# Performance work log

Hardware: AMD Instinct MI355X
Metric: run time of the kernel (lower is better)

The kernel has to match this reference:

```python
import jax, jax.numpy as jnp
import numpy as np

# ---- config (mirrors argparse-config of dnc_model) ----
T, B, IN = 64, 32, 64          # time-major input [T,B,IN]
N, Wd, R, NW = 512, 64, 4, 1   # memory_size, word_size, num_reads, num_writes
H, OUT = 256, 64               # controller hidden, output_size
CLIP = 20.0
EPS = 1e-6
IF = R*Wd + R + NW*Wd + NW + NW*Wd + NW*Wd + R + NW + NW + R*(1+2*NW)  # interface size = 471
CTRL_IN = IN + R*Wd


def setup_inputs() -> dict:
    key = jax.random.key(0)
    ks = jax.random.split(key, 6)
    g = lambda k, shape, s: (jax.random.normal(k, shape, jnp.float32) * s)
    return {
        "inputs": g(ks[0], (T, B, IN), 1.0),
        "Wx": g(ks[1], (CTRL_IN, 4*H), 0.05),
        "Wh": g(ks[2], (H, 4*H), 0.05),
        "b_lstm": jnp.zeros((4*H,), jnp.float32),
        "W_if": g(ks[3], (H, IF), 0.05),
        "b_if": jnp.zeros((IF,), jnp.float32),
        "W_out": g(ks[4], (H + R*Wd, OUT), 0.05),
        "b_out": jnp.zeros((OUT,), jnp.float32),
    }


def _clip(x):
    return jnp.clip(x, -CLIP, CLIP)


def _oneplus(x):
    return 1.0 + jax.nn.softplus(x)


def _content_weights(memory, keys, strengths):
    # memory [B,N,Wd], keys [B,K,Wd], strengths [B,K] -> softmax cosine weights [B,K,N]
    dot = jnp.einsum('bkw,bnw->bkn', keys, memory)
    mn = jnp.sqrt(jnp.sum(memory * memory, -1))          # [B,N]
    kn = jnp.sqrt(jnp.sum(keys * keys, -1))              # [B,K]
    sim = dot / (kn[..., None] * mn[:, None, :] + EPS)
    return jax.nn.softmax(sim * strengths[..., None], axis=-1)


def _allocation(usage):
    # usage [B,N] -> allocation weights [B,N] (sorted-free-list scheme)
    u = EPS + (1.0 - EPS) * usage
    idx = jnp.argsort(u, axis=-1)                        # ascending usage
    su = jnp.take_along_axis(u, idx, -1)
    cp = jnp.cumprod(su, axis=-1)
    excl = jnp.concatenate([jnp.ones_like(cp[:, :1]), cp[:, :-1]], -1)
    a_sorted = (1.0 - su) * excl
    inv = jnp.argsort(idx, axis=-1)
    return jnp.take_along_axis(a_sorted, inv, -1)


def _dnc_forward(inputs, Wx, Wh, b_lstm, W_if, b_if, W_out, b_out):
    eye = jnp.eye(N, dtype=inputs.dtype)

    def step(carry, x_t):
        h, c, mem, rw, ww_prev, link, prec, usage, reads = carry
        # ---- controller LSTM (prev read vectors fed in) ----
        ctrl_in = jnp.concatenate([x_t, reads.reshape(B, R*Wd)], -1)
        gates = ctrl_in @ Wx + h @ Wh + b_lstm
        ig, fg, gg, og = jnp.split(gates, 4, -1)
        c = jax.nn.sigmoid(fg) * c + jax.nn.sigmoid(ig) * jnp.tanh(gg)
        h = jax.nn.sigmoid(og) * jnp.tanh(c)
        hc, cc = _clip(h), _clip(c)
        # ---- interface vector ----
        itf = hc @ W_if + b_if
        off = 0
        read_keys = itf[:, off:off+R*Wd].reshape(B, R, Wd); off += R*Wd
        read_str = _oneplus(itf[:, off:off+R]); off += R
        write_keys = itf[:, off:off+NW*Wd].reshape(B, NW, Wd); off += NW*Wd
        write_str = _oneplus(itf[:, off:off+NW]); off += NW
        erase = jax.nn.sigmoid(itf[:, off:off+NW*Wd]).reshape(B, NW, Wd); off += NW*Wd
        write_vecs = itf[:, off:off+NW*Wd].reshape(B, NW, Wd); off += NW*Wd
        free_g = jax.nn.sigmoid(itf[:, off:off+R]); off += R
        alloc_g = jax.nn.sigmoid(itf[:, off:off+NW]); off += NW
        write_g = jax.nn.sigmoid(itf[:, off:off+NW]); off += NW
        modes = jax.nn.softmax(itf[:, off:off+R*(1+2*NW)].reshape(B, R, 1+2*NW), -1)
        bwd_mode = modes[..., :NW]
        fwd_mode = modes[..., NW:2*NW]
        content_mode = modes[..., 2*NW]
        # ---- usage update (uses prev write/read weights) ----
        u = usage + (1.0 - usage) * (1.0 - jnp.prod(1.0 - ww_prev, axis=1))
        psi = jnp.prod(1.0 - free_g[..., None] * rw, axis=1)
        usage = u * psi
        # ---- write weights: allocation + content ----
        allocs = []
        u_run = usage
        for hd in range(NW):
            a = _allocation(u_run)
            allocs.append(a)
            u_run = u_run + (1.0 - u_run) * (write_g[:, hd:hd+1] * alloc_g[:, hd:hd+1]) * a
        alloc = jnp.stack(allocs, 1)                      # [B,NW,N]
        wc = _content_weights(mem, write_keys, write_str) # [B,NW,N]
        ww = write_g[..., None] * (alloc_g[..., None] * alloc + (1.0 - alloc_g[..., None]) * wc)
        # ---- erase / add write ----
        erase_w = ww[..., None] * erase[:, :, None, :]    # [B,NW,N,Wd]
        mem = mem * jnp.prod(1.0 - erase_w, axis=1) + jnp.einsum('bhn,bhw->bnw', ww, write_vecs)
        # ---- temporal link + precedence ----
        w_i = ww[..., :, None]
        w_j = ww[..., None, :]
        link = (1.0 - w_i - w_j) * link + w_i * prec[..., None, :]
        link = link * (1.0 - eye)
        prec = (1.0 - ww.sum(-1, keepdims=True)) * prec + ww
        # ---- read weights: content + forward/backward linkage ----
        rc = _content_weights(mem, read_keys, read_str)   # [B,R,N]
        fw = jnp.einsum('bhij,brj->brhi', link, rw)       # forward  [B,R,NW,N]
        bw = jnp.einsum('bhji,brj->brhi', link, rw)       # backward [B,R,NW,N]
        rw = (content_mode[..., None] * rc
              + jnp.einsum('brh,brhn->brn', fwd_mode, fw)
              + jnp.einsum('brh,brhn->brn', bwd_mode, bw))
        reads = jnp.einsum('brn,bnw->brw', rw, mem)       # [B,R,Wd]
        out = _clip(jnp.concatenate([hc, reads.reshape(B, R*Wd)], -1) @ W_out + b_out)
        return (hc, cc, mem, rw, ww, link, prec, usage, reads), out

    z = jnp.zeros
    dt = inputs.dtype
    carry0 = (z((B, H), dt), z((B, H), dt), z((B, N, Wd), dt), z((B, R, N), dt),
              z((B, NW, N), dt), z((B, NW, N, N), dt), z((B, NW, N), dt),
              z((B, N), dt), z((B, R, Wd), dt))
    _, outs = jax.lax.scan(step, carry0, inputs)
    return outs  # [T, B, OUT]


def reference(inputs, Wx, Wh, b_lstm, W_if, b_if, W_out, b_out):
    return _dnc_forward(inputs, Wx, Wh, b_lstm, W_if, b_if, W_out, b_out)
```

## Files before the change

### kernel.cpp

```cpp
#include <hip/hip_runtime.h>
#include <math.h>

#define Tn 64
#define Bn 32
#define INn 64
#define Nn 512
#define WDn 64
#define Rn 4
#define Hn 256
#define G4H 1024
#define OUTn 64
#define IFn 471
#define CLIPV 20.0f
#define EPSV 1e-6f

#define OFF_RKEY 0
#define OFF_RSTR 256
#define OFF_WKEY 260
#define OFF_WSTR 324
#define OFF_ERASE 325
#define OFF_WVEC 389
#define OFF_FREE 453
#define OFF_AG 457
#define OFF_WG 458
#define OFF_MODES 459

__device__ float S_h[2][Bn][Hn];
__device__ float S_c[2][Bn][Hn];
__device__ float S_gates[2][Bn][G4H];
__device__ float S_mem[Bn][Nn][WDn];
__device__ float S_rw[Bn][Rn][Nn];
__device__ float S_ww[2][Bn][Nn];
__device__ float S_link[Bn][Nn][Nn];
__device__ float S_prec[2][Bn][Nn];
__device__ float S_usage[2][Bn][Nn];
__device__ float S_reads[Bn][Rn][WDn];
__device__ float S_itf[Bn][IFn];
__device__ float S_rc[Bn][Rn][Nn];
__device__ float S_fw[Bn][Rn][Nn];
__device__ float S_bwp[Bn][8][Rn*Nn];
__device__ float S_sumww[Bn];
__device__ unsigned int g_ww[Bn];
__device__ unsigned int g_rc[Bn];
__device__ unsigned int g_ld[Bn];
__device__ unsigned int g_fin;

__device__ __forceinline__ float sigm(float x){ return 1.f/(1.f+expf(-x)); }
__device__ __forceinline__ float clipv(float x){ return fminf(fmaxf(x,-CLIPV),CLIPV); }
__device__ __forceinline__ float oneplusf(float x){
  float sp = (x > 0.f) ? (x + log1pf(expf(-x))) : log1pf(expf(x));
  return 1.f + sp;
}
__device__ __forceinline__ float wredsum(float v){
  #pragma unroll
  for (int o=32;o>0;o>>=1) v += __shfl_xor(v,o,64);
  return v;
}
__device__ __forceinline__ float bredsum(float v, volatile float* scr){
  v = wredsum(v);
  if ((threadIdx.x & 63) == 0) scr[threadIdx.x >> 6] = v;
  __syncthreads();
  float s = scr[0];
  #pragma unroll
  for (int i=1;i<8;i++) s += scr[i];
  __syncthreads();
  return s;
}
__device__ __forceinline__ float bredmax(float v, volatile float* scr){
  #pragma unroll
  for (int o=32;o>0;o>>=1) v = fmaxf(v,__shfl_xor(v,o,64));
  if ((threadIdx.x & 63) == 0) scr[threadIdx.x >> 6] = v;
  __syncthreads();
  float m = scr[0];
  #pragma unroll
  for (int i=1;i<8;i++) m = fmaxf(m, scr[i]);
  __syncthreads();
  return m;
}
__device__ __forceinline__ void sig_release(unsigned int* flag){
  __builtin_amdgcn_fence(__ATOMIC_RELEASE, "agent");
  __hip_atomic_fetch_add(flag, 1u, __ATOMIC_RELAXED, __HIP_MEMORY_SCOPE_AGENT);
}
__device__ __forceinline__ void spin_until(unsigned int* flag, unsigned int target){
  while (__hip_atomic_load(flag, __ATOMIC_RELAXED, __HIP_MEMORY_SCOPE_AGENT) < target)
    __builtin_amdgcn_s_sleep(8);
}

extern "C" __global__ void __launch_bounds__(256)
k_init(){
  size_t g = (size_t)blockIdx.x*256 + threadIdx.x;
  size_t stride = (size_t)gridDim.x*256;
  float* lk = &S_link[0][0][0];
  for (size_t i=g; i<(size_t)Bn*Nn*Nn; i+=stride) lk[i]=0.f;
  float* mm = &S_mem[0][0][0];
  for (size_t i=g; i<(size_t)Bn*Nn*WDn; i+=stride) mm[i]=0.f;
  float* rr = &S_rw[0][0][0];
  for (size_t i=g; i<(size_t)Bn*Rn*Nn; i+=stride) rr[i]=0.f;
  float* rd = &S_reads[0][0][0];
  for (size_t i=g; i<(size_t)Bn*Rn*WDn; i+=stride) rd[i]=0.f;
  for (size_t i=g; i<(size_t)2*Bn*Nn; i+=stride){
    S_ww[0][0][i]=0.f; S_prec[0][0][i]=0.f; S_usage[0][0][i]=0.f;
  }
  for (size_t i=g; i<(size_t)2*Bn*Hn; i+=stride){
    S_h[0][0][i]=0.f; S_c[0][0][i]=0.f;
  }
  if (blockIdx.x==0){
    if (threadIdx.x < Bn){ g_ww[threadIdx.x]=0u; g_rc[threadIdx.x]=0u; g_ld[threadIdx.x]=0u; }
    if (threadIdx.x == 0) g_fin=0u;
  }
}

struct ShG { float ctrl[Bn][65]; };

__device__ __forceinline__ void gates_core(ShG& sg, int tn, int jt,
        const float* __restrict__ xin, const float* __restrict__ Wx,
        const float* __restrict__ Wh, const float* __restrict__ b_lstm){
  const int tid = threadIdx.x, lane = tid & 63, wvi = tid >> 6;
  const int j = jt*64 + lane;
  const int hp = (tn+1)&1;
  const int b0 = wvi*4;
  float bias = b_lstm[j];
  float a0=bias, a1=bias, a2=bias, a3=bias;
  for (int c=0;c<9;++c){
    #pragma unroll
    for (int u=0;u<4;u++){
      int e = u*512 + tid;
      int b2 = e >> 6, kk = e & 63;
      float v;
      if (c==0)       v = xin[((size_t)tn*Bn + b2)*INn + kk];
      else if (c<5)   v = ((const float*)S_reads[b2])[(c-1)*64 + kk];
      else            v = S_h[hp][b2][(c-5)*64 + kk];
      sg.ctrl[b2][kk] = v;
    }
    __syncthreads();
    const float* wb = (c<5) ? (Wx + (size_t)(c*64)*G4H + j)
                            : (Wh + (size_t)((c-5)*64)*G4H + j);
    #pragma unroll
    for (int kk=0;kk<64;kk++){
      float wv = wb[(size_t)kk*G4H];
      a0 += sg.ctrl[b0+0][kk]*wv;
      a1 += sg.ctrl[b0+1][kk]*wv;
      a2 += sg.ctrl[b0+2][kk]*wv;
      a3 += sg.ctrl[b0+3][kk]*wv;
    }
    __syncthreads();
  }
  const int gs = tn&1;
  S_gates[gs][b0+0][j]=a0;
  S_gates[gs][b0+1][j]=a1;
  S_gates[gs][b0+2][j]=a2;
  S_gates[gs][b0+3][j]=a3;
}

extern "C" __global__ void __launch_bounds__(512)
k_gates_pro(const float* __restrict__ xin, const float* __restrict__ Wx,
            const float* __restrict__ Wh, const float* __restrict__ b_lstm){
  __shared__ ShG sg;
  gates_core(sg, 0, blockIdx.x, xin, Wx, Wh, b_lstm);
}

struct ShA {
  float hc[Hn];
  float itf[IFn];
  unsigned long long keys[Nn];
  float alloc[Nn];
  float sim[Nn];
  float rsim[Rn][Nn];
  float tile[64][65];
  float wkey[WDn];
  float rk[Rn][WDn];
  float er[WDn];
  float wv[WDn];
  float red[8];
  float knw, knr[Rn], betar[Rn];
};
struct ShL {
  float ww[Nn];
  float prec[Nn];
  float rw[Rn][Nn];
  float bwp4[4][Rn][Nn];
};
struct ShF {
  float fw[Rn][Nn];
  float bw[Rn][Nn];
  float rc[Rn][Nn];
  float modes[Rn][4];
  float part[8][Rn][WDn];
  float vin[512];
};
union ShU { ShA a; ShL l; ShF f; ShG g; };

extern "C" __global__ void __launch_bounds__(512, 4)
k_step(int t, const float* __restrict__ xin,
       const float* __restrict__ Wx, const float* __restrict__ Wh,
       const float* __restrict__ b_lstm,
       const float* __restrict__ W_if, const float* __restrict__ b_if,
       const float* __restrict__ W_out, const float* __restrict__ b_out,
       float* __restrict__ outp){
  __shared__ ShU sh;
  const int tid = threadIdx.x;
  const int lane = tid & 63, wvi = tid >> 6;
  const int bid = blockIdx.x;
  const int cur = t&1, prev = cur^1;

  if (bid < 32){
    const int b = bid;
    if (tid < Hn){
      int h = tid;
      float g0=S_gates[cur][b][h],     g1=S_gates[cur][b][Hn+h];
      float g2=S_gates[cur][b][2*Hn+h],g3=S_gates[cur][b][3*Hn+h];
      float cold = S_c[prev][b][h];
      float cn = sigm(g1)*cold + sigm(g0)*tanhf(g2);
      float hn = sigm(g3)*tanhf(cn);
      float hcv = clipv(hn);
      S_c[cur][b][h] = clipv(cn);
      S_h[cur][b][h] = hcv;
      sh.a.hc[h] = hcv;
    }
    __syncthreads();
    if (tid < IFn){
      float acc = b_if[tid];
      for (int k=0;k<Hn;k+=8){
        float s = 0.f;
        #pragma unroll
        for (int u=0;u<8;u++) s += sh.a.hc[k+u]*W_if[(size_t)(k+u)*IFn + tid];
        acc += s;
      }
      sh.a.itf[tid] = acc;
      S_itf[b][tid] = acc;
    }
    __syncthreads();
    if (tid < WDn){
      sh.a.wkey[tid] = sh.a.itf[OFF_WKEY+tid];
      sh.a.er[tid]   = sigm(sh.a.itf[OFF_ERASE+tid]);
      sh.a.wv[tid]   = sh.a.itf[OFF_WVEC+tid];
    } else if (tid < WDn + Rn*WDn){
      int k2 = tid - WDn;
      sh.a.rk[k2>>6][k2&63] = sh.a.itf[OFF_RKEY + k2];
    }
    {
      float fg0=sigm(sh.a.itf[OFF_FREE+0]), fg1=sigm(sh.a.itf[OFF_FREE+1]);
      float fg2=sigm(sh.a.itf[OFF_FREE+2]), fg3=sigm(sh.a.itf[OFF_FREE+3]);
      int n = tid;
      float uu = S_usage[prev][b][n], wwp = S_ww[prev][b][n];
      float u = uu + (1.f-uu)*wwp;
      float psi = (1.f - fg0*S_rw[b][0][n])*(1.f - fg1*S_rw[b][1][n])
                * (1.f - fg2*S_rw[b][2][n])*(1.f - fg3*S_rw[b][3][n]);
      float un = u*psi;
      S_usage[cur][b][n] = un;
      float v = EPSV + (1.f-EPSV)*un;
      sh.a.keys[n] = ((unsigned long long)__float_as_uint(v) << 32) | (unsigned)n;
    }
    __syncthreads();
    if (wvi==0){
      float kv = sh.a.wkey[lane];
      float s2 = wredsum(kv*kv);
      if (lane==0) sh.a.knw = sqrtf(s2);
    } else if (wvi<=4){
      int r = wvi-1;
      float kv = sh.a.rk[r][lane];
      float s2 = wredsum(kv*kv);
      if (lane==0) sh.a.knr[r] = sqrtf(s2);
    } else if (wvi==5 && lane<4){
      sh.a.betar[lane] = oneplusf(sh.a.itf[OFF_RSTR+lane]);
    }
    {
      unsigned long long myk = sh.a.keys[tid];
      float prod = 1.f;
      for (int j=0;j<Nn;j+=8){
        #pragma unroll
        for (int u=0;u<8;u++){
          unsigned long long kj = sh.a.keys[j+u];
          float uj = __uint_as_float((unsigned)(kj>>32));
          prod *= (kj < myk) ? uj : 1.f;
        }
      }
      float myu = __uint_as_float((unsigned)(myk>>32));
      sh.a.alloc[tid] = (1.f - myu)*prod;
    }
    __syncthreads();
    float betaw = oneplusf(sh.a.itf[OFF_WSTR]);
    for (int tile=0;tile<8;tile++){
      #pragma unroll
      for (int u=0;u<8;u++){
        int e = u*512 + tid;
        int nn = e>>6, w = e&63;
        sh.a.tile[nn][w] = S_mem[b][tile*64+nn][w];
      }
      __syncthreads();
      {
        int nn = tid>>3, qq = tid&7;
        float d=0.f, nrm=0.f;
        #pragma unroll
        for (int i=0;i<8;i++){
          int w = qq*8+i;
          float m = sh.a.tile[nn][w];
          d += m*sh.a.wkey[w]; nrm += m*m;
        }
        #pragma unroll
        for (int o=1;o<8;o<<=1){ d += __shfl_xor(d,o,64); nrm += __shfl_xor(nrm,o,64); }
        if (qq==0){
          int n = tile*64+nn;
          sh.a.sim[n] = betaw * d / (sh.a.knw*sqrtf(nrm) + EPSV);
        }
      }
      __syncthreads();
    }
    {
      float v = sh.a.sim[tid];
      float mx = bredmax(v, sh.a.red);
      float e = expf(v - mx);
      float ssum = bredsum(e, sh.a.red);
      float wc = e/ssum;
      float ag = sigm(sh.a.itf[OFF_AG]);
      float wg = sigm(sh.a.itf[OFF_WG]);
      float wwv = wg*(ag*sh.a.alloc[tid] + (1.f-ag)*wc);
      S_ww[cur][b][tid] = wwv;
      float wsum = bredsum(wwv, sh.a.red);
      if (tid==0) S_sumww[b] = wsum;
      sh.a.alloc[tid] = wwv;
    }
    __syncthreads();
    if (tid==0) sig_release(&g_ww[b]);
    for (int tile=0;tile<8;tile++){
      #pragma unroll
      for (int u=0;u<8;u++){
        int e = u*512 + tid;
        int nn = e>>6, w = e&63;
        int n = tile*64+nn;
        float m = S_mem[b][n][w];
        float wwn = sh.a.alloc[n];
        m = m*(1.f - wwn*sh.a.er[w]) + wwn*sh.a.wv[w];
        S_mem[b][n][w] = m;
        sh.a.tile[nn][w] = m;
      }
      __syncthreads();
      {
        int nn = tid>>3, qq = tid&7;
        float a0=0.f,a1=0.f,a2=0.f,a3=0.f,nrm=0.f;
        #pragma unroll
        for (int i=0;i<8;i++){
          int w = qq*8+i;
          float m = sh.a.tile[nn][w];
          a0 += m*sh.a.rk[0][w]; a1 += m*sh.a.rk[1][w];
          a2 += m*sh.a.rk[2][w]; a3 += m*sh.a.rk[3][w];
          nrm += m*m;
        }
        #pragma unroll
        for (int o=1;o<8;o<<=1){
          a0 += __shfl_xor(a0,o,64); a1 += __shfl_xor(a1,o,64);
          a2 += __shfl_xor(a2,o,64); a3 += __shfl_xor(a3,o,64);
          nrm += __shfl_xor(nrm,o,64);
        }
        if (qq==0){
          int n = tile*64+nn;
          float mn = sqrtf(nrm);
          sh.a.rsim[0][n] = sh.a.betar[0]*a0/(sh.a.knr[0]*mn + EPSV);
          sh.a.rsim[1][n] = sh.a.betar[1]*a1/(sh.a.knr[1]*mn + EPSV);
          sh.a.rsim[2][n] = sh.a.betar[2]*a2/(sh.a.knr[2]*mn + EPSV);
          sh.a.rsim[3][n] = sh.a.betar[3]*a3/(sh.a.knr[3]*mn + EPSV);
        }
      }
      __syncthreads();
    }
    for (int r=0;r<Rn;r++){
      float v = sh.a.rsim[r][tid];
      float mx = bredmax(v, sh.a.red);
      float e = expf(v - mx);
      float ssum = bredsum(e, sh.a.red);
      S_rc[b][r][tid] = e/ssum;
    }
    __syncthreads();
    if (tid==0) sig_release(&g_rc[b]);

  } else if (bid < 288){
    const int idx = bid - 32;
    const int b = idx >> 3, ch = idx & 7;
    const int i0 = ch*64;
    if (tid==0){
      spin_until(&g_ww[b], (unsigned)(t+1));
      __builtin_amdgcn_fence(__ATOMIC_ACQUIRE, "agent");
    }
    __syncthreads();
    sh.l.ww[tid]   = S_ww[cur][b][tid];
    sh.l.prec[tid] = S_prec[prev][b][tid];
    for (int k=tid;k<Rn*Nn;k+=512) ((float*)sh.l.rw)[k] = ((const float*)S_rw[b])[k];
    __syncthreads();
    float sumww = S_sumww[b];
    float wj[2][4], pj[2][4], rj[4][2][4];
    #pragma unroll
    for (int jjc=0;jjc<2;jjc++){
      float4 w4 = ((const float4*)sh.l.ww)[jjc*64+lane];
      float4 p4 = ((const float4*)sh.l.prec)[jjc*64+lane];
      wj[jjc][0]=w4.x; wj[jjc][1]=w4.y; wj[jjc][2]=w4.z; wj[jjc][3]=w4.w;
      pj[jjc][0]=p4.x; pj[jjc][1]=p4.y; pj[jjc][2]=p4.z; pj[jjc][3]=p4.w;
      #pragma unroll
      for (int r=0;r<4;r++){
        float4 r4 = ((const float4*)sh.l.rw[r])[jjc*64+lane];
        rj[r][jjc][0]=r4.x; rj[r][jjc][1]=r4.y; rj[r][jjc][2]=r4.z; rj[r][jjc][3]=r4.w;
      }
    }
    float bwa[4][2][4];
    #pragma unroll
    for (int r=0;r<4;r++)
      #pragma unroll
      for (int jjc=0;jjc<2;jjc++)
        #pragma unroll
        for (int s=0;s<4;s++) bwa[r][jjc][s]=0.f;
    for (int rr=0;rr<8;rr++){
      const int i = i0 + wvi*8 + rr;
      float wi = sh.l.ww[i];
      float ci = 1.f - wi;
      float ri[4] = {sh.l.rw[0][i], sh.l.rw[1][i], sh.l.rw[2][i], sh.l.rw[3][i]};
      float f[4] = {0.f,0.f,0.f,0.f};
      float4* lrow4 = (float4*)(&S_link[b][i][0]);
      #pragma unroll
      for (int jjc=0;jjc<2;jjc++){
        float4 L4 = lrow4[jjc*64+lane];
        float Ls[4] = {L4.x, L4.y, L4.z, L4.w};
        #pragma unroll
        for (int s=0;s<4;s++){
          float Ln = (ci - wj[jjc][s])*Ls[s] + wi*pj[jjc][s];
          int j = jjc*256 + lane*4 + s;
          Ln = (j==i) ? 0.f : Ln;
          Ls[s] = Ln;
          #pragma unroll
          for (int r=0;r<4;r++){
            f[r] += Ln*rj[r][jjc][s];
            bwa[r][jjc][s] += Ln*ri[r];
          }
        }
        float4 Lo; Lo.x=Ls[0]; Lo.y=Ls[1]; Lo.z=Ls[2]; Lo.w=Ls[3];
        lrow4[jjc*64+lane] = Lo;
      }
      #pragma unroll
      for (int r=0;r<4;r++){
        float fr = wredsum(f[r]);
        if (lane==0) S_fw[b][r][i] = fr;
      }
    }
    if (wvi < 4){
      #pragma unroll
      for (int r=0;r<4;r++)
        #pragma unroll
        for (int jjc=0;jjc<2;jjc++){
          float4 v4; v4.x=bwa[r][jjc][0]; v4.y=bwa[r][jjc][1]; v4.z=bwa[r][jjc][2]; v4.w=bwa[r][jjc][3];
          ((float4*)sh.l.bwp4[wvi][r])[jjc*64+lane] = v4;
        }
    }
    __syncthreads();
    if (wvi >= 4){
      int v = wvi-4;
      #pragma unroll
      for (int r=0;r<4;r++)
        #pragma unroll
        for (int jjc=0;jjc<2;jjc++){
          float4 v4 = ((float4*)sh.l.bwp4[v][r])[jjc*64+lane];
          v4.x+=bwa[r][jjc][0]; v4.y+=bwa[r][jjc][1]; v4.z+=bwa[r][jjc][2]; v4.w+=bwa[r][jjc][3];
          ((float4*)sh.l.bwp4[v][r])[jjc*64+lane] = v4;
        }
    }
    __syncthreads();
    for (int k=tid;k<Rn*Nn;k+=512){
      float s = ((float*)sh.l.bwp4[0])[k] + ((float*)sh.l.bwp4[1])[k]
              + ((float*)sh.l.bwp4[2])[k] + ((float*)sh.l.bwp4[3])[k];
      S_bwp[b][ch][k] = s;
    }
    if (tid < 64){
      int j = i0 + tid;
      S_prec[cur][b][j] = (1.f - sumww)*sh.l.prec[j] + sh.l.ww[j];
    }
    __syncthreads();
    if (tid==0) sig_release(&g_ld[b]);

  } else if (bid < 320){
    const int b = bid - 288;
    if (tid==0){
      spin_until(&g_ld[b], 8u*(unsigned)(t+1));
      spin_until(&g_rc[b], (unsigned)(t+1));
      __builtin_amdgcn_fence(__ATOMIC_ACQUIRE, "agent");
    }
    __syncthreads();
    for (int k=tid;k<Rn*Nn;k+=512){
      ((float*)sh.f.fw)[k] = ((const float*)S_fw[b])[k];
      float sbw = 0.f;
      #pragma unroll
      for (int ch=0;ch<8;ch++) sbw += S_bwp[b][ch][k];
      ((float*)sh.f.bw)[k] = sbw;
      ((float*)sh.f.rc)[k] = ((const float*)S_rc[b])[k];
    }
    if (tid < 4){
      int r = tid;
      float m0 = S_itf[b][OFF_MODES + r*3 + 0];
      float m1 = S_itf[b][OFF_MODES + r*3 + 1];
      float m2 = S_itf[b][OFF_MODES + r*3 + 2];
      float mx = fmaxf(m0,fmaxf(m1,m2));
      float e0=expf(m0-mx), e1=expf(m1-mx), e2=expf(m2-mx);
      float si = e0+e1+e2;
      sh.f.modes[r][0]=e0/si; sh.f.modes[r][1]=e1/si; sh.f.modes[r][2]=e2/si;
    }
    __syncthreads();
    for (int k=tid;k<Rn*Nn;k+=512){
      int r = k>>9, n = k&511;
      float v = sh.f.modes[r][2]*sh.f.rc[r][n] + sh.f.modes[r][1]*sh.f.fw[r][n]
              + sh.f.modes[r][0]*sh.f.bw[r][n];
      sh.f.rc[r][n] = v;
      S_rw[b][r][n] = v;
    }
    __syncthreads();
    {
      float a0=0.f,a1=0.f,a2=0.f,a3=0.f;
      #pragma unroll 4
      for (int nn=0;nn<64;nn++){
        int n = wvi*64+nn;
        float m = S_mem[b][n][lane];
        a0 += sh.f.rc[0][n]*m; a1 += sh.f.rc[1][n]*m;
        a2 += sh.f.rc[2][n]*m; a3 += sh.f.rc[3][n]*m;
      }
      sh.f.part[wvi][0][lane]=a0; sh.f.part[wvi][1][lane]=a1;
      sh.f.part[wvi][2][lane]=a2; sh.f.part[wvi][3][lane]=a3;
    }
    __syncthreads();
    if (tid < 256){
      int r = tid>>6, w = tid&63;
      float sv = 0.f;
      #pragma unroll
      for (int v=0;v<8;v++) sv += sh.f.part[v][r][w];
      S_reads[b][r][w] = sv;
      sh.f.vin[256+tid] = sv;
      sh.f.vin[tid] = S_h[cur][b][tid];
    }
    __syncthreads();
    {
      int qq = tid>>6, o = tid&63;
      float sacc = 0.f;
      for (int k2=qq*64;k2<qq*64+64;k2+=8){
        #pragma unroll
        for (int u=0;u<8;u++) sacc += sh.f.vin[k2+u]*W_out[(size_t)(k2+u)*OUTn + o];
      }
      sh.f.part[qq][0][o] = sacc;
    }
    __syncthreads();
    if (tid < 64){
      float sv = b_out[tid];
      #pragma unroll
      for (int qq=0;qq<8;qq++) sv += sh.f.part[qq][0][tid];
      outp[((size_t)t*Bn + b)*OUTn + tid] = clipv(sv);
    }
    __syncthreads();
    if (tid==0) sig_release(&g_fin);

  } else {
    if (t+1 >= Tn) return;
    const int jt = bid - 320;
    if (tid==0){
      spin_until(&g_fin, 32u*(unsigned)(t+1));
      __builtin_amdgcn_fence(__ATOMIC_ACQUIRE, "agent");
    }
    __syncthreads();
    gates_core(sh.g, t+1, jt, xin, Wx, Wh, b_lstm);
  }
}

extern "C" void kernel_launch(void* const* d_in, const int* in_sizes, int n_in,
                              void* d_out, int out_size, void* d_ws, size_t ws_size,
                              hipStream_t stream){
  (void)in_sizes; (void)n_in; (void)d_ws; (void)ws_size; (void)out_size;
  const float* xin = (const float*)d_in[0];
  const float* Wx  = (const float*)d_in[1];
  const float* Wh  = (const float*)d_in[2];
  const float* bl  = (const float*)d_in[3];
  const float* Wif = (const float*)d_in[4];
  const float* bif = (const float*)d_in[5];
  const float* Wo  = (const float*)d_in[6];
  const float* bo  = (const float*)d_in[7];
  hipLaunchKernelGGL(k_init, dim3(1024), dim3(256), 0, stream);
  hipLaunchKernelGGL(k_gates_pro, dim3(16), dim3(512), 0, stream, xin, Wx, Wh, bl);
  for (int t=0; t<Tn; ++t){
    hipLaunchKernelGGL(k_step, dim3(336), dim3(512), 0, stream,
                       t, xin, Wx, Wh, bl, Wif, bif, Wo, bo, (float*)d_out);
  }
}
```

Before: 7.154 ms.

## Move memory write and read-content weights to final blocks, overlap gate precompute

The memory erase/write update and the read-content similarity softmax move out of the per-batch controller blocks into the final read blocks. Those blocks now start right after the write weights are published and run concurrently with the linkage blocks, instead of serialising behind them. The next-step gate blocks begin the x and h parts of the LSTM matmul as soon as a new h-published flag is set, deferring only the read-vector part until the step finishes. This shortens the critical path per step at the cost of more flags and more work in the read blocks. Flags are padded to separate cache lines, the spin sleep is shortened, and the W_if loop unroll is increased.

```diff
diff --git a/kernel.cpp b/kernel.cpp
--- a/kernel.cpp
+++ b/kernel.cpp
@@ -36,14 +36,13 @@
 __device__ float S_usage[2][Bn][Nn];
 __device__ float S_reads[Bn][Rn][WDn];
 __device__ float S_itf[Bn][IFn];
-__device__ float S_rc[Bn][Rn][Nn];
 __device__ float S_fw[Bn][Rn][Nn];
 __device__ float S_bwp[Bn][8][Rn*Nn];
 __device__ float S_sumww[Bn];
-__device__ unsigned int g_ww[Bn];
-__device__ unsigned int g_rc[Bn];
-__device__ unsigned int g_ld[Bn];
-__device__ unsigned int g_fin;
+__device__ unsigned int g_hh[16];
+__device__ unsigned int g_ww[Bn][16];
+__device__ unsigned int g_ld[Bn][16];
+__device__ unsigned int g_fin[16];
 
 __device__ __forceinline__ float sigm(float x){ return 1.f/(1.f+expf(-x)); }
 __device__ __forceinline__ float clipv(float x){ return fminf(fmaxf(x,-CLIPV),CLIPV); }
@@ -83,7 +82,14 @@
 }
 __device__ __forceinline__ void spin_until(unsigned int* flag, unsigned int target){
   while (__hip_atomic_load(flag, __ATOMIC_RELAXED, __HIP_MEMORY_SCOPE_AGENT) < target)
-    __builtin_amdgcn_s_sleep(8);
+    __builtin_amdgcn_s_sleep(4);
+}
+__device__ __forceinline__ void wait_acq1(unsigned int* f, unsigned int tgt){
+  if (threadIdx.x==0){
+    spin_until(f, tgt);
+    __builtin_amdgcn_fence(__ATOMIC_ACQUIRE, "agent");
+  }
+  __syncthreads();
 }
 
 extern "C" __global__ void __launch_bounds__(256)
@@ -105,19 +111,55 @@
     S_h[0][0][i]=0.f; S_c[0][0][i]=0.f;
   }
   if (blockIdx.x==0){
-    if (threadIdx.x < Bn){ g_ww[threadIdx.x]=0u; g_rc[threadIdx.x]=0u; g_ld[threadIdx.x]=0u; }
-    if (threadIdx.x == 0) g_fin=0u;
+    for (int i=threadIdx.x; i<16; i+=256){ g_hh[i]=0u; g_fin[i]=0u; }
+    for (int i=threadIdx.x; i<Bn*16; i+=256){
+      ((unsigned int*)g_ww)[i]=0u; ((unsigned int*)g_ld)[i]=0u;
+    }
   }
 }
 
 struct ShG { float ctrl[Bn][65]; };
-
-__device__ __forceinline__ void gates_core(ShG& sg, int tn, int jt,
-        const float* __restrict__ xin, const float* __restrict__ Wx,
-        const float* __restrict__ Wh, const float* __restrict__ b_lstm){
+struct ShA {
+  float hc[Hn];
+  float itf[IFn];
+  unsigned long long keys[Nn];
+  float alloc[Nn];
+  float sim[Nn];
+  float tile[64][65];
+  float wkey[WDn];
+  float red[8];
+  float knw;
+};
+struct ShL {
+  float ww[Nn];
+  float prec[Nn];
+  float rw[Rn][Nn];
+  float bwp4[4][Rn][Nn];
+};
+struct ShF {
+  float er[WDn];
+  float wv[WDn];
+  float rk[Rn][WDn];
+  float betar[Rn];
+  float knr[Rn];
+  float modes[Rn][4];
+  float ww[Nn];
+  float tile[64][65];
+  float rsim[Rn][Nn];
+  float fw[Rn][Nn];
+  float bw[Rn][Nn];
+  float part[8][Rn][WDn];
+  float vin[512];
+  float red[8];
+};
+union ShU { ShA a; ShL l; ShF f; ShG g; };
+
+extern "C" __global__ void __launch_bounds__(512)
+k_gates_pro(const float* __restrict__ xin, const float* __restrict__ Wx,
+            const float* __restrict__ Wh, const float* __restrict__ b_lstm){
+  __shared__ ShG sg;
   const int tid = threadIdx.x, lane = tid & 63, wvi = tid >> 6;
-  const int j = jt*64 + lane;
-  const int hp = (tn+1)&1;
+  const int j = blockIdx.x*64 + lane;
   const int b0 = wvi*4;
   float bias = b_lstm[j];
   float a0=bias, a1=bias, a2=bias, a3=bias;
@@ -127,9 +169,9 @@
       int e = u*512 + tid;
       int b2 = e >> 6, kk = e & 63;
       float v;
-      if (c==0)       v = xin[((size_t)tn*Bn + b2)*INn + kk];
-      else if (c<5)   v = ((const float*)S_reads[b2])[(c-1)*64 + kk];
-      else            v = S_h[hp][b2][(c-5)*64 + kk];
+      if (c==0)       v = xin[(size_t)b2*INn + kk];
+      else if (c<5)   v = 0.f;
+      else            v = 0.f;
       sg.ctrl[b2][kk] = v;
     }
     __syncthreads();
@@ -145,50 +187,11 @@
     }
     __syncthreads();
   }
-  const int gs = tn&1;
-  S_gates[gs][b0+0][j]=a0;
-  S_gates[gs][b0+1][j]=a1;
-  S_gates[gs][b0+2][j]=a2;
-  S_gates[gs][b0+3][j]=a3;
-}
-
-extern "C" __global__ void __launch_bounds__(512)
-k_gates_pro(const float* __restrict__ xin, const float* __restrict__ Wx,
-            const float* __restrict__ Wh, const float* __restrict__ b_lstm){
-  __shared__ ShG sg;
-  gates_core(sg, 0, blockIdx.x, xin, Wx, Wh, b_lstm);
-}
-
-struct ShA {
-  float hc[Hn];
-  float itf[IFn];
-  unsigned long long keys[Nn];
-  float alloc[Nn];
-  float sim[Nn];
-  float rsim[Rn][Nn];
-  float tile[64][65];
-  float wkey[WDn];
-  float rk[Rn][WDn];
-  float er[WDn];
-  float wv[WDn];
-  float red[8];
-  float knw, knr[Rn], betar[Rn];
-};
-struct ShL {
-  float ww[Nn];
-  float prec[Nn];
-  float rw[Rn][Nn];
-  float bwp4[4][Rn][Nn];
-};
-struct ShF {
-  float fw[Rn][Nn];
-  float bw[Rn][Nn];
-  float rc[Rn][Nn];
-  float modes[Rn][4];
-  float part[8][Rn][WDn];
-  float vin[512];
-};
-union ShU { ShA a; ShL l; ShF f; ShG g; };
+  S_gates[0][b0+0][j]=a0;
+  S_gates[0][b0+1][j]=a1;
+  S_gates[0][b0+2][j]=a2;
+  S_gates[0][b0+3][j]=a3;
+}
 
 extern "C" __global__ void __launch_bounds__(512, 4)
 k_step(int t, const float* __restrict__ xin,
@@ -218,26 +221,20 @@
       sh.a.hc[h] = hcv;
     }
     __syncthreads();
+    if (tid==0) sig_release(&g_hh[0]);
     if (tid < IFn){
       float acc = b_if[tid];
-      for (int k=0;k<Hn;k+=8){
+      for (int k=0;k<Hn;k+=16){
         float s = 0.f;
         #pragma unroll
-        for (int u=0;u<8;u++) s += sh.a.hc[k+u]*W_if[(size_t)(k+u)*IFn + tid];
+        for (int u=0;u<16;u++) s += sh.a.hc[k+u]*W_if[(size_t)(k+u)*IFn + tid];
         acc += s;
       }
       sh.a.itf[tid] = acc;
       S_itf[b][tid] = acc;
     }
     __syncthreads();
-    if (tid < WDn){
-      sh.a.wkey[tid] = sh.a.itf[OFF_WKEY+tid];
-      sh.a.er[tid]   = sigm(sh.a.itf[OFF_ERASE+tid]);
-      sh.a.wv[tid]   = sh.a.itf[OFF_WVEC+tid];
-    } else if (tid < WDn + Rn*WDn){
-      int k2 = tid - WDn;
-      sh.a.rk[k2>>6][k2&63] = sh.a.itf[OFF_RKEY + k2];
-    }
+    if (tid < WDn) sh.a.wkey[tid] = sh.a.itf[OFF_WKEY+tid];
     {
       float fg0=sigm(sh.a.itf[OFF_FREE+0]), fg1=sigm(sh.a.itf[OFF_FREE+1]);
       float fg2=sigm(sh.a.itf[OFF_FREE+2]), fg3=sigm(sh.a.itf[OFF_FREE+3]);
@@ -256,13 +253,6 @@
       float kv = sh.a.wkey[lane];
       float s2 = wredsum(kv*kv);
       if (lane==0) sh.a.knw = sqrtf(s2);
-    } else if (wvi<=4){
-      int r = wvi-1;
-      float kv = sh.a.rk[r][lane];
-      float s2 = wredsum(kv*kv);
-      if (lane==0) sh.a.knr[r] = sqrtf(s2);
-    } else if (wvi==5 && lane<4){
-      sh.a.betar[lane] = oneplusf(sh.a.itf[OFF_RSTR+lane]);
     }
     {
       unsigned long long myk = sh.a.keys[tid];
@@ -318,70 +308,15 @@
       S_ww[cur][b][tid] = wwv;
       float wsum = bredsum(wwv, sh.a.red);
       if (tid==0) S_sumww[b] = wsum;
-      sh.a.alloc[tid] = wwv;
-    }
-    __syncthreads();
-    if (tid==0) sig_release(&g_ww[b]);
-    for (int tile=0;tile<8;tile++){
-      #pragma unroll
-      for (int u=0;u<8;u++){
-        int e = u*512 + tid;
-        int nn = e>>6, w = e&63;
-        int n = tile*64+nn;
-        float m = S_mem[b][n][w];
-        float wwn = sh.a.alloc[n];
-        m = m*(1.f - wwn*sh.a.er[w]) + wwn*sh.a.wv[w];
-        S_mem[b][n][w] = m;
-        sh.a.tile[nn][w] = m;
-      }
-      __syncthreads();
-      {
-        int nn = tid>>3, qq = tid&7;
-        float a0=0.f,a1=0.f,a2=0.f,a3=0.f,nrm=0.f;
-        #pragma unroll
-        for (int i=0;i<8;i++){
-          int w = qq*8+i;
-          float m = sh.a.tile[nn][w];
-          a0 += m*sh.a.rk[0][w]; a1 += m*sh.a.rk[1][w];
-          a2 += m*sh.a.rk[2][w]; a3 += m*sh.a.rk[3][w];
-          nrm += m*m;
-        }
-        #pragma unroll
-        for (int o=1;o<8;o<<=1){
-          a0 += __shfl_xor(a0,o,64); a1 += __shfl_xor(a1,o,64);
-          a2 += __shfl_xor(a2,o,64); a3 += __shfl_xor(a3,o,64);
-          nrm += __shfl_xor(nrm,o,64);
-        }
-        if (qq==0){
-          int n = tile*64+nn;
-          float mn = sqrtf(nrm);
-          sh.a.rsim[0][n] = sh.a.betar[0]*a0/(sh.a.knr[0]*mn + EPSV);
-          sh.a.rsim[1][n] = sh.a.betar[1]*a1/(sh.a.knr[1]*mn + EPSV);
-          sh.a.rsim[2][n] = sh.a.betar[2]*a2/(sh.a.knr[2]*mn + EPSV);
-          sh.a.rsim[3][n] = sh.a.betar[3]*a3/(sh.a.knr[3]*mn + EPSV);
-        }
-      }
-      __syncthreads();
-    }
-    for (int r=0;r<Rn;r++){
-      float v = sh.a.rsim[r][tid];
-      float mx = bredmax(v, sh.a.red);
-      float e = expf(v - mx);
-      float ssum = bredsum(e, sh.a.red);
-      S_rc[b][r][tid] = e/ssum;
-    }
-    __syncthreads();
-    if (tid==0) sig_release(&g_rc[b]);
+    }
+    __syncthreads();
+    if (tid==0) sig_release(&g_ww[b][0]);
 
   } else if (bid < 288){
     const int idx = bid - 32;
     const int b = idx >> 3, ch = idx & 7;
     const int i0 = ch*64;
-    if (tid==0){
-      spin_until(&g_ww[b], (unsigned)(t+1));
-      __builtin_amdgcn_fence(__ATOMIC_ACQUIRE, "agent");
-    }
-    __syncthreads();
+    wait_acq1(&g_ww[b][0], (unsigned)(t+1));
     sh.l.ww[tid]   = S_ww[cur][b][tid];
     sh.l.prec[tid] = S_prec[prev][b][tid];
     for (int k=tid;k<Rn*Nn;k+=512) ((float*)sh.l.rw)[k] = ((const float*)S_rw[b])[k];
@@ -471,26 +406,22 @@
       S_prec[cur][b][j] = (1.f - sumww)*sh.l.prec[j] + sh.l.ww[j];
     }
     __syncthreads();
-    if (tid==0) sig_release(&g_ld[b]);
+    if (tid==0) sig_release(&g_ld[b][0]);
 
   } else if (bid < 320){
     const int b = bid - 288;
-    if (tid==0){
-      spin_until(&g_ld[b], 8u*(unsigned)(t+1));
-      spin_until(&g_rc[b], (unsigned)(t+1));
-      __builtin_amdgcn_fence(__ATOMIC_ACQUIRE, "agent");
-    }
-    __syncthreads();
-    for (int k=tid;k<Rn*Nn;k+=512){
-      ((float*)sh.f.fw)[k] = ((const float*)S_fw[b])[k];
-      float sbw = 0.f;
-      #pragma unroll
-      for (int ch=0;ch<8;ch++) sbw += S_bwp[b][ch][k];
-      ((float*)sh.f.bw)[k] = sbw;
-      ((float*)sh.f.rc)[k] = ((const float*)S_rc[b])[k];
-    }
-    if (tid < 4){
-      int r = tid;
+    wait_acq1(&g_ww[b][0], (unsigned)(t+1));
+    if (tid < WDn){
+      sh.f.er[tid] = sigm(S_itf[b][OFF_ERASE+tid]);
+      sh.f.wv[tid] = S_itf[b][OFF_WVEC+tid];
+    } else if (tid < WDn + Rn*WDn){
+      int k2 = tid - WDn;
+      sh.f.rk[k2>>6][k2&63] = S_itf[b][OFF_RKEY + k2];
+    } else if (tid < WDn + Rn*WDn + Rn){
+      int r = tid - (WDn+Rn*WDn);
+      sh.f.betar[r] = oneplusf(S_itf[b][OFF_RSTR + r]);
+    } else if (tid >= 384 && tid < 384+Rn){
+      int r = tid - 384;
       float m0 = S_itf[b][OFF_MODES + r*3 + 0];
       float m1 = S_itf[b][OFF_MODES + r*3 + 1];
       float m2 = S_itf[b][OFF_MODES + r*3 + 2];
@@ -499,12 +430,76 @@
       float si = e0+e1+e2;
       sh.f.modes[r][0]=e0/si; sh.f.modes[r][1]=e1/si; sh.f.modes[r][2]=e2/si;
     }
+    sh.f.ww[tid] = S_ww[cur][b][tid];
+    __syncthreads();
+    if (wvi < 4){
+      float kv = sh.f.rk[wvi][lane];
+      float s2 = wredsum(kv*kv);
+      if (lane==0) sh.f.knr[wvi] = sqrtf(s2);
+    }
+    for (int tile=0;tile<8;tile++){
+      #pragma unroll
+      for (int u=0;u<8;u++){
+        int e = u*512 + tid;
+        int nn = e>>6, w = e&63;
+        int n = tile*64+nn;
+        float m = S_mem[b][n][w];
+        float wwn = sh.f.ww[n];
+        m = m*(1.f - wwn*sh.f.er[w]) + wwn*sh.f.wv[w];
+        S_mem[b][n][w] = m;
+        sh.f.tile[nn][w] = m;
+      }
+      __syncthreads();
+      {
+        int nn = tid>>3, qq = tid&7;
+        float a0=0.f,a1=0.f,a2=0.f,a3=0.f,nrm=0.f;
+        #pragma unroll
+        for (int i=0;i<8;i++){
+          int w = qq*8+i;
+          float m = sh.f.tile[nn][w];
+          a0 += m*sh.f.rk[0][w]; a1 += m*sh.f.rk[1][w];
+          a2 += m*sh.f.rk[2][w]; a3 += m*sh.f.rk[3][w];
+          nrm += m*m;
+        }
+        #pragma unroll
+        for (int o=1;o<8;o<<=1){
+          a0 += __shfl_xor(a0,o,64); a1 += __shfl_xor(a1,o,64);
+          a2 += __shfl_xor(a2,o,64); a3 += __shfl_xor(a3,o,64);
+          nrm += __shfl_xor(nrm,o,64);
+        }
+        if (qq==0){
+          int n = tile*64+nn;
+          float mn = sqrtf(nrm);
+          sh.f.rsim[0][n] = sh.f.betar[0]*a0/(sh.f.knr[0]*mn + EPSV);
+          sh.f.rsim[1][n] = sh.f.betar[1]*a1/(sh.f.knr[1]*mn + EPSV);
+          sh.f.rsim[2][n] = sh.f.betar[2]*a2/(sh.f.knr[2]*mn + EPSV);
+          sh.f.rsim[3][n] = sh.f.betar[3]*a3/(sh.f.knr[3]*mn + EPSV);
+        }
+      }
+      __syncthreads();
+    }
+    for (int r=0;r<Rn;r++){
+      float v = sh.f.rsim[r][tid];
+      float mx = bredmax(v, sh.f.red);
+      float e = expf(v - mx);
+      float ssum = bredsum(e, sh.f.red);
+      sh.f.rsim[r][tid] = e/ssum;
+    }
+    __syncthreads();
+    wait_acq1(&g_ld[b][0], 8u*(unsigned)(t+1));
+    for (int k=tid;k<Rn*Nn;k+=512){
+      ((float*)sh.f.fw)[k] = ((const float*)S_fw[b])[k];
+      float sbw = 0.f;
+      #pragma unroll
+      for (int ch=0;ch<8;ch++) sbw += S_bwp[b][ch][k];
+      ((float*)sh.f.bw)[k] = sbw;
+    }
     __syncthreads();
     for (int k=tid;k<Rn*Nn;k+=512){
       int r = k>>9, n = k&511;
-      float v = sh.f.modes[r][2]*sh.f.rc[r][n] + sh.f.modes[r][1]*sh.f.fw[r][n]
+      float v = sh.f.modes[r][2]*sh.f.rsim[r][n] + sh.f.modes[r][1]*sh.f.fw[r][n]
               + sh.f.modes[r][0]*sh.f.bw[r][n];
-      sh.f.rc[r][n] = v;
+      sh.f.rsim[r][n] = v;
       S_rw[b][r][n] = v;
     }
     __syncthreads();
@@ -514,8 +509,8 @@
       for (int nn=0;nn<64;nn++){
         int n = wvi*64+nn;
         float m = S_mem[b][n][lane];
-        a0 += sh.f.rc[0][n]*m; a1 += sh.f.rc[1][n]*m;
-        a2 += sh.f.rc[2][n]*m; a3 += sh.f.rc[3][n]*m;
+        a0 += sh.f.rsim[0][n]*m; a1 += sh.f.rsim[1][n]*m;
+        a2 += sh.f.rsim[2][n]*m; a3 += sh.f.rsim[3][n]*m;
       }
       sh.f.part[wvi][0][lane]=a0; sh.f.part[wvi][1][lane]=a1;
       sh.f.part[wvi][2][lane]=a2; sh.f.part[wvi][3][lane]=a3;
@@ -548,17 +543,65 @@
       outp[((size_t)t*Bn + b)*OUTn + tid] = clipv(sv);
     }
     __syncthreads();
-    if (tid==0) sig_release(&g_fin);
+    if (tid==0) sig_release(&g_fin[0]);
 
   } else {
     if (t+1 >= Tn) return;
     const int jt = bid - 320;
-    if (tid==0){
-      spin_until(&g_fin, 32u*(unsigned)(t+1));
-      __builtin_amdgcn_fence(__ATOMIC_ACQUIRE, "agent");
-    }
-    __syncthreads();
-    gates_core(sh.g, t+1, jt, xin, Wx, Wh, b_lstm);
+    const int j = jt*64 + lane;
+    const int b0 = wvi*4;
+    const int hp = cur;
+    float bias = b_lstm[j];
+    float a0=bias, a1=bias, a2=bias, a3=bias;
+    wait_acq1(&g_hh[0], 32u*(unsigned)(t+1));
+    for (int c=0;c<5;++c){
+      #pragma unroll
+      for (int u=0;u<4;u++){
+        int e = u*512 + tid;
+        int b2 = e >> 6, kk = e & 63;
+        float v;
+        if (c==0) v = xin[((size_t)(t+1)*Bn + b2)*INn + kk];
+        else      v = S_h[hp][b2][(c-1)*64 + kk];
+        sh.g.ctrl[b2][kk] = v;
+      }
+      __syncthreads();
+      const float* wb = (c==0) ? (Wx + j)
+                               : (Wh + (size_t)((c-1)*64)*G4H + j);
+      #pragma unroll
+      for (int kk=0;kk<64;kk++){
+        float wv = wb[(size_t)kk*G4H];
+        a0 += sh.g.ctrl[b0+0][kk]*wv;
+        a1 += sh.g.ctrl[b0+1][kk]*wv;
+        a2 += sh.g.ctrl[b0+2][kk]*wv;
+        a3 += sh.g.ctrl[b0+3][kk]*wv;
+      }
+      __syncthreads();
+    }
+    wait_acq1(&g_fin[0], 32u*(unsigned)(t+1));
+    for (int c=0;c<4;++c){
+      #pragma unroll
+      for (int u=0;u<4;u++){
+        int e = u*512 + tid;
+        int b2 = e >> 6, kk = e & 63;
+        sh.g.ctrl[b2][kk] = ((const float*)S_reads[b2])[c*64 + kk];
+      }
+      __syncthreads();
+      const float* wb = Wx + (size_t)(INn + c*64)*G4H + j;
+      #pragma unroll
+      for (int kk=0;kk<64;kk++){
+        float wv = wb[(size_t)kk*G4H];
+        a0 += sh.g.ctrl[b0+0][kk]*wv;
+        a1 += sh.g.ctrl[b0+1][kk]*wv;
+        a2 += sh.g.ctrl[b0+2][kk]*wv;
+        a3 += sh.g.ctrl[b0+3][kk]*wv;
+      }
+      __syncthreads();
+    }
+    const int gs = (t+1)&1;
+    S_gates[gs][b0+0][j]=a0;
+    S_gates[gs][b0+1][j]=a1;
+    S_gates[gs][b0+2][j]=a2;
+    S_gates[gs][b0+3][j]=a3;
   }
 }
 
```

New measurement: 6.347 ms. 1.13x faster.
